# Kernel optimization log

Measured on AMD Instinct MI355X. Metric: run time of the kernel, lower is better.

The kernel has to match this reference:

```python
import jax, jax.numpy as jnp
import numpy as np

N = 100000   # nodes
E = 1000000  # edges
G = 1024     # graphs
S = 128      # subgraphs (super-graphs)
NODE = 64    # node feature dim
EDGE = 32    # edge feature dim
H = 64       # hidden size
OUT = 32     # output classes
L = 3        # num GIN layers
BN_EPS = 1e-5


def setup_inputs() -> dict:
    key = jax.random.key(0)
    ks = jax.random.split(key, 32)
    p = lambda k, shape: jax.random.normal(k, shape, jnp.float32) * 0.05
    inp = {
        "x": jax.random.normal(ks[0], (N, NODE), jnp.float32),
        "edge_index": jax.random.randint(ks[1], (2, E), 0, N),
        "edge_attr": jax.random.normal(ks[2], (E, EDGE), jnp.float32),
        "batch": jnp.sort(jax.random.randint(ks[3], (N,), 0, G)),
        "weights": jax.random.uniform(ks[4], (G, 1), jnp.float32, 0.1, 1.0),
        "subgraph_batch": jnp.sort(jax.random.randint(ks[5], (G,), 0, S)),
        # per-layer GINConv params (node_size == hidden_size so layers stack)
        "be_w1": p(ks[6], (L, EDGE, H)), "be_b1": p(ks[7], (L, H)),
        "be_w2": p(ks[8], (L, H, H)),   "be_b2": p(ks[9], (L, H)),
        "mlp_w1": p(ks[10], (L, H, H)), "mlp_b1": p(ks[11], (L, H)),
        "mlp_w2": p(ks[12], (L, H, H)), "mlp_b2": p(ks[13], (L, H)),
        "eps": jnp.zeros((L,), jnp.float32),
        "bn_gamma": jnp.ones((L, H), jnp.float32),
        "bn_beta": jnp.zeros((L, H), jnp.float32),
        "fc0_w": p(ks[14], (L * H, H)), "fc0_b": p(ks[15], (H,)),
        "fc1_w": p(ks[16], (H, H)),     "fc1_b": p(ks[17], (H,)),
        "fc2_w": p(ks[18], (H, H)),     "fc2_b": p(ks[19], (H,)),
        "pred_w": p(ks[20], (H, OUT)),  "pred_b": p(ks[21], (OUT,)),
    }
    return inp


def reference(x, edge_index, edge_attr, batch, weights, subgraph_batch,
              be_w1, be_b1, be_w2, be_b2, mlp_w1, mlp_b1, mlp_w2, mlp_b2,
              eps, bn_gamma, bn_beta, fc0_w, fc0_b, fc1_w, fc1_b,
              fc2_w, fc2_b, pred_w, pred_b):
    src, dst = edge_index[0], edge_index[1]
    n = x.shape[0]
    h = x
    xs = []
    for l in range(be_w1.shape[0]):
        # bond encoder: Linear -> ReLU -> Linear  [E, H]
        e = jnp.maximum(edge_attr @ be_w1[l] + be_b1[l], 0.0) @ be_w2[l] + be_b2[l]
        # message: relu(x_j + edge_emb), aggregate: scatter-add to target nodes
        msg = jnp.maximum(h[src] + e, 0.0)                      # [E, H]
        agg = jax.ops.segment_sum(msg, dst, num_segments=n)     # [N, H]
        z = (1.0 + eps[l]) * h + agg
        # update MLP: Linear -> ReLU -> Linear, then outer ReLU
        z = jnp.maximum(z @ mlp_w1[l] + mlp_b1[l], 0.0) @ mlp_w2[l] + mlp_b2[l]
        z = jnp.maximum(z, 0.0)
        # BatchNorm over nodes (training-mode batch statistics, biased var)
        mu = z.mean(axis=0)
        var = z.var(axis=0)
        z = (z - mu) * jax.lax.rsqrt(var + BN_EPS) * bn_gamma[l] + bn_beta[l]
        h = z
        xs.append(z)
    hc = jnp.concatenate(xs, axis=-1)                           # [N, L*H]
    g_num = weights.shape[0]
    cnt = jax.ops.segment_sum(jnp.ones((n,), hc.dtype), batch, num_segments=g_num)
    g = jax.ops.segment_sum(hc, batch, num_segments=g_num) / jnp.maximum(cnt, 1.0)[:, None]
    g = jnp.maximum(g @ fc0_w + fc0_b, 0.0) * weights           # [G, H]
    s = jax.ops.segment_sum(g, subgraph_batch, num_segments=S)  # [S, H]
    norm = jax.ops.segment_sum(weights, subgraph_batch, num_segments=S)
    s = s / jnp.maximum(norm, 1e-12)
    s = jnp.maximum(s @ fc1_w + fc1_b, 0.0)
    s = jnp.maximum(s @ fc2_w + fc2_b, 0.0)
    return s @ pred_w + pred_b                                  # [S, OUT]
```

## Files before the change

### kernel.cpp

```cpp
#include <hip/hip_runtime.h>

#define NN 100000
#define NE 1000000
#define NG 1024
#define NSG 128
#define EF 32
#define HH 64
#define NOUT 32
#define NL 3
#define NWAVE (NE / 64)
#define NGRP_N (NN / 16)

typedef __attribute__((ext_vector_type(8))) short bf16x8;
typedef __attribute__((ext_vector_type(4))) float f32x4;

#define EMIDX(row, c) ((row) * 64 + (((c) + (row) * 4) & 63))

__device__ __forceinline__ float bcastf(float v, int l) {
    return __int_as_float(__builtin_amdgcn_readlane(__float_as_int(v), l));
}

__device__ __forceinline__ short f2bf(float x) {
    unsigned u = __float_as_uint(x);
    u += 0x7FFFu + ((u >> 16) & 1u);
    return (short)(u >> 16);
}

__device__ __forceinline__ float bf2f(short h) {
    return __uint_as_float(((unsigned)(unsigned short)h) << 16);
}

__device__ __forceinline__ void wave_lds_sync() {
    __builtin_amdgcn_wave_barrier();
    asm volatile("s_waitcnt lgkmcnt(0)" ::: "memory");
    __builtin_amdgcn_wave_barrier();
}

__device__ __forceinline__ void gld16(const float* g, float* l) {
    __builtin_amdgcn_global_load_lds(
        (const __attribute__((address_space(1))) void*)g,
        (__attribute__((address_space(3))) void*)l, 16, 0, 0);
}

#define WAITVM_(n) asm volatile("s_waitcnt vmcnt(" #n ")" ::: "memory")
#define WAITVM(n) WAITVM_(n)

__global__ void prep_kernel(const int* __restrict__ batch, const int* __restrict__ sgb,
                            const float* __restrict__ w,
                            float* __restrict__ cnt, float* __restrict__ norm) {
    int i = blockIdx.x * blockDim.x + threadIdx.x;
    if (i < NN) atomicAdd(&cnt[batch[i]], 1.0f);
    if (i < NG) atomicAdd(&norm[sgb[i]], w[i]);
}

__global__ void hist_kernel(const int* __restrict__ eidx, int* __restrict__ off) {
    int e = blockIdx.x * 256 + threadIdx.x;
    if (e < NE) atomicAdd(&off[eidx[NE + e]], 1);
}

__global__ void scan1(int* __restrict__ off, int* __restrict__ bsum) {
    __shared__ int s[256];
    const int i = blockIdx.x * 256 + threadIdx.x;
    const int v = (i < NN) ? off[i] : 0;
    s[threadIdx.x] = v; __syncthreads();
    for (int d = 1; d < 256; d <<= 1) {
        const int t = (threadIdx.x >= d) ? s[threadIdx.x - d] : 0;
        __syncthreads(); s[threadIdx.x] += t; __syncthreads();
    }
    if (i < NN) off[i] = s[threadIdx.x] - v;
    if (threadIdx.x == 255) bsum[blockIdx.x] = s[255];
}

__global__ void scan2(int* __restrict__ bsum, int nb) {
    __shared__ int s[512];
    const int v = (threadIdx.x < nb) ? bsum[threadIdx.x] : 0;
    s[threadIdx.x] = v; __syncthreads();
    for (int d = 1; d < 512; d <<= 1) {
        const int t = (threadIdx.x >= d) ? s[threadIdx.x - d] : 0;
        __syncthreads(); s[threadIdx.x] += t; __syncthreads();
    }
    if (threadIdx.x < nb) bsum[threadIdx.x] = s[threadIdx.x] - v;
}

__global__ void scan3(int* __restrict__ off, const int* __restrict__ bsum) {
    const int i = blockIdx.x * 256 + threadIdx.x;
    if (i < NN) off[i] += bsum[blockIdx.x];
}

__global__ void scatter_kernel(const int* __restrict__ eidx, int* __restrict__ off,
                               int* __restrict__ perm_s, int* __restrict__ src_s,
                               int* __restrict__ dst_s) {
    int e = blockIdx.x * 256 + threadIdx.x;
    if (e < NE) {
        const int d = eidx[NE + e];
        const int p = atomicAdd(&off[d], 1);
        perm_s[p] = e;
        src_s[p]  = eidx[e];
        dst_s[p]  = d;
    }
}

__global__ __launch_bounds__(256, 4) void edge_mfma(
    const float* __restrict__ hin,
    const float* __restrict__ eattr,
    const int*   __restrict__ perm_s,
    const int*   __restrict__ src_s,
    const int*   __restrict__ dst_s,
    const float* __restrict__ w1,
    const float* __restrict__ b1,
    const float* __restrict__ w2,
    const float* __restrict__ b2,
    float*       __restrict__ agg)
{
    __shared__ float ldsall[4][2560];
    const int lane = threadIdx.x & 63;
    const int wv   = threadIdx.x >> 6;
    const int col  = lane & 15;
    const int quad = lane >> 4;
    float* EM = &ldsall[wv][0];
    short* T  = (short*)EM;
    float* HG = &ldsall[wv][1024];
    float* EA = &ldsall[wv][2048];

    const int wid = __builtin_amdgcn_readfirstlane(
        (blockIdx.x * 256 + (int)threadIdx.x) >> 6);
    if (wid >= NWAVE) return;
    const int ebase = wid * 64;

    bf16x8 B1f[4];
    #pragma unroll
    for (int nt = 0; nt < 4; ++nt)
        #pragma unroll
        for (int j = 0; j < 8; ++j)
            B1f[nt][j] = f2bf(w1[(quad * 8 + j) * HH + nt * 16 + col]);
    bf16x8 B2f[2][4];
    #pragma unroll
    for (int ks = 0; ks < 2; ++ks)
        #pragma unroll
        for (int nt = 0; nt < 4; ++nt)
            #pragma unroll
            for (int j = 0; j < 8; ++j)
                B2f[ks][nt][j] = f2bf(w2[(ks * 32 + quad * 8 + j) * HH + nt * 16 + col]);
    float b1v[4], b2v[4];
    #pragma unroll
    for (int nt = 0; nt < 4; ++nt) {
        b1v[nt] = b1[nt * 16 + col];
        b2v[nt] = b2[nt * 16 + col];
    }

    const int sv_all = src_s[ebase + lane];
    const int dv_all = dst_s[ebase + lane];
    const int pe_all = perm_s[ebase + lane];

    const int ea_srcchunk = (lane & 7) ^ ((lane >> 3) & 7);
    const int ea_subrow   = lane >> 3;
    const int hg_subrow   = lane >> 4;
    const int hg_off      = (lane & 15) * 4;

    #define ISSUE_EA(g)                                                        \
        {                                                                      \
            _Pragma("unroll")                                                  \
            for (int b = 0; b < 2; ++b) {                                      \
                const int srow = (g) * 16 + b * 8 + ea_subrow;                 \
                const int pe   = __shfl(pe_all, srow, 64);                     \
                gld16(eattr + (size_t)pe * EF + ea_srcchunk * 4,               \
                      EA + b * 256);                                           \
            }                                                                  \
        }
    #define ISSUE_HG(g)                                                        \
        {                                                                      \
            _Pragma("unroll")                                                  \
            for (int b = 0; b < 4; ++b) {                                      \
                const int srow = (g) * 16 + b * 4 + hg_subrow;                 \
                const int s    = __shfl(sv_all, srow, 64);                     \
                gld16(hin + (size_t)s * HH + hg_off, HG + b * 256);            \
            }                                                                  \
        }

    WAITVM(0);
    __builtin_amdgcn_sched_barrier(0);

    ISSUE_EA(0);
    ISSUE_HG(0);

    int   cur = -1;
    float acc = 0.0f;

    #pragma unroll
    for (int gi = 0; gi < 4; ++gi) {
        WAITVM(4);
        __builtin_amdgcn_sched_barrier(0);

        const int sbase = (2 * quad) ^ (col & 6);
        const float4 fa = *(const float4*)&EA[col * 32 + sbase * 4];
        const float4 fb = *(const float4*)&EA[col * 32 + sbase * 4 + 4];
        const bool odd = (col & 1);
        const float4 lo = odd ? fb : fa;
        const float4 hi = odd ? fa : fb;
        bf16x8 A1;
        A1[0] = f2bf(lo.x); A1[1] = f2bf(lo.y); A1[2] = f2bf(lo.z); A1[3] = f2bf(lo.w);
        A1[4] = f2bf(hi.x); A1[5] = f2bf(hi.y); A1[6] = f2bf(hi.z); A1[7] = f2bf(hi.w);
        wave_lds_sync();
        if (gi < 3) ISSUE_EA(gi + 1);

        #pragma unroll
        for (int nt = 0; nt < 4; ++nt) {
            f32x4 C = {0.f, 0.f, 0.f, 0.f};
            C = __builtin_amdgcn_mfma_f32_16x16x32_bf16(A1, B1f[nt], C, 0, 0, 0);
            #pragma unroll
            for (int r = 0; r < 4; ++r) {
                const float tv = fmaxf(C[r] + b1v[nt], 0.0f);
                T[(quad * 4 + r) * 72 + nt * 16 + col] = f2bf(tv);
            }
        }
        wave_lds_sync();

        bf16x8 A2_0 = *(const bf16x8*)&T[col * 72 + 0  + quad * 8];
        bf16x8 A2_1 = *(const bf16x8*)&T[col * 72 + 32 + quad * 8];
        wave_lds_sync();

        #pragma unroll
        for (int nt = 0; nt < 4; ++nt) {
            f32x4 C = {0.f, 0.f, 0.f, 0.f};
            C = __builtin_amdgcn_mfma_f32_16x16x32_bf16(A2_0, B2f[0][nt], C, 0, 0, 0);
            C = __builtin_amdgcn_mfma_f32_16x16x32_bf16(A2_1, B2f[1][nt], C, 0, 0, 0);
            #pragma unroll
            for (int r = 0; r < 4; ++r)
                EM[EMIDX(quad * 4 + r, nt * 16 + col)] = C[r] + b2v[nt];
        }
        wave_lds_sync();

        if (gi < 3) { WAITVM(2); } else { WAITVM(0); }
        __builtin_amdgcn_sched_barrier(0);

        #pragma unroll
        for (int e2 = 0; e2 < 16; ++e2) {
            const int d = __builtin_amdgcn_readlane(dv_all, gi * 16 + e2);
            const float msg = fmaxf(HG[e2 * 64 + lane] + EM[EMIDX(e2, lane)], 0.0f);
            if (d != cur) {
                if (cur >= 0) atomicAdd(&agg[(size_t)cur * HH + lane], acc);
                acc = 0.0f; cur = d;
            }
            acc += msg;
        }
        wave_lds_sync();
        if (gi < 3) ISSUE_HG(gi + 1);
    }
    if (cur >= 0) atomicAdd(&agg[(size_t)cur * HH + lane], acc);
    #undef ISSUE_EA
    #undef ISSUE_HG
}

__global__ __launch_bounds__(256, 3) void node_mfma(
    const float* __restrict__ hin,
    float*       agg,
    const float* __restrict__ w1, const float* __restrict__ b1,
    const float* __restrict__ w2, const float* __restrict__ b2,
    const float* __restrict__ epsp,
    float*       __restrict__ stats)
{
    __shared__ short wt[4][64 * 72];
    __shared__ float em[4][16 * 64];

    const int tid = threadIdx.x;
    for (int idx = tid; idx < HH * HH; idx += 256) {
        const int k = idx >> 6, n = idx & 63;
        {
            const float w = w1[idx];
            const short h = f2bf(w);
            wt[0][n * 72 + k] = h;
            wt[1][n * 72 + k] = f2bf(w - bf2f(h));
        }
        {
            const float w = w2[idx];
            const short h = f2bf(w);
            wt[2][n * 72 + k] = h;
            wt[3][n * 72 + k] = f2bf(w - bf2f(h));
        }
    }
    __syncthreads();

    const int lane = tid & 63;
    const int wv   = tid >> 6;
    const int col  = lane & 15;
    const int quad = lane >> 4;
    float* EM = em[wv];
    const float epsv = 1.0f + epsp[0];
    const int wid = blockIdx.x * 4 + wv;

    float b1v[4], b2v[4];
    #pragma unroll
    for (int nt = 0; nt < 4; ++nt) {
        b1v[nt] = b1[nt * 16 + col];
        b2v[nt] = b2[nt * 16 + col];
    }

    float s1 = 0.0f, s2 = 0.0f;

    #pragma unroll 1
    for (int gi = 0; gi < 4; ++gi) {
        const int grp = wid * 4 + gi;
        if (grp >= NGRP_N) break;
        const int n0  = grp * 16;
        const int row = n0 + col;

        bf16x8 Ah[2], Al[2];
        #pragma unroll
        for (int ks = 0; ks < 2; ++ks) {
            const float* hp = hin + (size_t)row * HH + ks * 32 + quad * 8;
            const float* gp = agg + (size_t)row * HH + ks * 32 + quad * 8;
            const float4 h0 = *(const float4*)hp;
            const float4 h1 = *(const float4*)(hp + 4);
            const float4 g0 = *(const float4*)gp;
            const float4 g1 = *(const float4*)(gp + 4);
            float z[8];
            z[0] = fmaf(epsv, h0.x, g0.x); z[1] = fmaf(epsv, h0.y, g0.y);
            z[2] = fmaf(epsv, h0.z, g0.z); z[3] = fmaf(epsv, h0.w, g0.w);
            z[4] = fmaf(epsv, h1.x, g1.x); z[5] = fmaf(epsv, h1.y, g1.y);
            z[6] = fmaf(epsv, h1.z, g1.z); z[7] = fmaf(epsv, h1.w, g1.w);
            #pragma unroll
            for (int j = 0; j < 8; ++j) {
                const short h = f2bf(z[j]);
                Ah[ks][j] = h;
                Al[ks][j] = f2bf(z[j] - bf2f(h));
            }
        }

        #pragma unroll
        for (int nt = 0; nt < 4; ++nt) {
            f32x4 C = {0.f, 0.f, 0.f, 0.f};
            #pragma unroll
            for (int ks = 0; ks < 2; ++ks) {
                const int wo = (nt * 16 + col) * 72 + ks * 32 + quad * 8;
                const bf16x8 Bh = *(const bf16x8*)&wt[0][wo];
                const bf16x8 Bl = *(const bf16x8*)&wt[1][wo];
                C = __builtin_amdgcn_mfma_f32_16x16x32_bf16(Ah[ks], Bh, C, 0, 0, 0);
                C = __builtin_amdgcn_mfma_f32_16x16x32_bf16(Al[ks], Bh, C, 0, 0, 0);
                C = __builtin_amdgcn_mfma_f32_16x16x32_bf16(Ah[ks], Bl, C, 0, 0, 0);
            }
            #pragma unroll
            for (int r = 0; r < 4; ++r)
                EM[EMIDX(quad * 4 + r, nt * 16 + col)] = fmaxf(C[r] + b1v[nt], 0.0f);
        }
        wave_lds_sync();

        bf16x8 Th[2], Tl[2];
        #pragma unroll
        for (int ks = 0; ks < 2; ++ks) {
            const int c0 = (ks * 32 + quad * 8 + col * 4) & 63;
            const float* tp = &EM[col * 64 + c0];
            const float4 t0 = *(const float4*)tp;
            const int c1 = (ks * 32 + quad * 8 + 4 + col * 4) & 63;
            const float4 t1 = *(const float4*)&EM[col * 64 + c1];
            float tz[8] = {t0.x, t0.y, t0.z, t0.w, t1.x, t1.y, t1.z, t1.w};
            #pragma unroll
            for (int j = 0; j < 8; ++j) {
                const short h = f2bf(tz[j]);
                Th[ks][j] = h;
                Tl[ks][j] = f2bf(tz[j] - bf2f(h));
            }
        }
        wave_lds_sync();

        #pragma unroll
        for (int nt = 0; nt < 4; ++nt) {
            f32x4 C = {0.f, 0.f, 0.f, 0.f};
            #pragma unroll
            for (int ks = 0; ks < 2; ++ks) {
                const int wo = (nt * 16 + col) * 72 + ks * 32 + quad * 8;
                const bf16x8 Bh = *(const bf16x8*)&wt[2][wo];
                const bf16x8 Bl = *(const bf16x8*)&wt[3][wo];
                C = __builtin_amdgcn_mfma_f32_16x16x32_bf16(Th[ks], Bh, C, 0, 0, 0);
                C = __builtin_amdgcn_mfma_f32_16x16x32_bf16(Tl[ks], Bh, C, 0, 0, 0);
                C = __builtin_amdgcn_mfma_f32_16x16x32_bf16(Th[ks], Bl, C, 0, 0, 0);
            }
            #pragma unroll
            for (int r = 0; r < 4; ++r)
                EM[EMIDX(quad * 4 + r, nt * 16 + col)] = fmaxf(C[r] + b2v[nt], 0.0f);
        }
        wave_lds_sync();

        #pragma unroll 4
        for (int e2 = 0; e2 < 16; ++e2) {
            const float val = EM[EMIDX(e2, lane)];
            agg[(size_t)(n0 + e2) * HH + lane] = val;
            s1 += val;
            s2 += val * val;
        }
        wave_lds_sync();
    }
    atomicAdd(&stats[lane], s1);
    atomicAdd(&stats[64 + lane], s2);
}

#define CHUNK 32
__global__ void bn_apply(
    const float* __restrict__ v, const float* __restrict__ stats,
    const float* __restrict__ gamma, const float* __restrict__ beta,
    const int* __restrict__ batch,
    float* __restrict__ hout, float* __restrict__ pooled, int layer)
{
    const int lane = threadIdx.x & 63;
    const int wv   = (blockIdx.x * blockDim.x + threadIdx.x) >> 6;
    const int n0   = wv * CHUNK;
    if (n0 >= NN) return;
    const int n1 = min(n0 + CHUNK, NN);
    const float mu  = stats[lane] * (1.0f / NN);
    const float var = stats[64 + lane] * (1.0f / NN) - mu * mu;
    const float rs  = 1.0f / sqrtf(var + 1e-5f);
    const float ga = gamma[lane],       be = beta[lane];
    float acc = 0.0f;
    int cur = batch[n0];
    for (int n = n0; n < n1; ++n) {
        const int b = batch[n];
        const float z = (v[(size_t)n * HH + lane] - mu) * rs * ga + be;
        hout[(size_t)n * HH + lane] = z;
        if (b != cur) {
            atomicAdd(&pooled[(size_t)cur * (NL * HH) + layer * HH + lane], acc);
            acc = 0.0f; cur = b;
        }
        acc += z;
    }
    atomicAdd(&pooled[(size_t)cur * (NL * HH) + layer * HH + lane], acc);
}

__global__ __launch_bounds__(256, 1) void graph_kernel(
    const float* __restrict__ pooled, const float* __restrict__ cnt,
    const float* __restrict__ fc0_w, const float* __restrict__ fc0_b,
    const float* __restrict__ wts, const int* __restrict__ sgb,
    float* __restrict__ s_acc)
{
    __shared__ float w[NL * HH * HH];
    for (int i = threadIdx.x; i < NL * HH * HH; i += blockDim.x) w[i] = fc0_w[i];
    __syncthreads();
    const int lane = threadIdx.x & 63;
    const int g = blockIdx.x * 4 + (threadIdx.x >> 6);
    if (g >= NG) return;
    const float inv = 1.0f / fmaxf(cnt[g], 1.0f);
    float acc = fc0_b[lane];
    #pragma unroll
    for (int c = 0; c < NL; ++c) {
        const float a = pooled[g * (NL * HH) + c * HH + lane] * inv;
        #pragma unroll
        for (int k = 0; k < HH; ++k)
            acc = fmaf(bcastf(a, k), w[(c * HH + k) * HH + lane], acc);
    }
    const float og = fmaxf(acc, 0.0f) * wts[g];
    atomicAdd(&s_acc[sgb[g] * HH + lane], og);
}

__global__ __launch_bounds__(256, 1) void final_kernel(
    const float* __restrict__ s_acc, const float* __restrict__ norm,
    const float* __restrict__ fc1_w, const float* __restrict__ fc1_b,
    const float* __restrict__ fc2_w, const float* __restrict__ fc2_b,
    const float* __restrict__ pw, const float* __restrict__ pb,
    float* __restrict__ out)
{
    const int lane = threadIdx.x & 63;
    const int s = blockIdx.x * 4 + (threadIdx.x >> 6);
    if (s >= NSG) return;
    const float xv = s_acc[s * HH + lane] / fmaxf(norm[s], 1e-12f);
    float u = fc1_b[lane];
    #pragma unroll
    for (int k = 0; k < HH; ++k) u = fmaf(bcastf(xv, k), fc1_w[k * HH + lane], u);
    u = fmaxf(u, 0.0f);
    float v = fc2_b[lane];
    #pragma unroll
    for (int k = 0; k < HH; ++k) v = fmaf(bcastf(u, k), fc2_w[k * HH + lane], v);
    v = fmaxf(v, 0.0f);
    float o = pb[lane & 31];
    #pragma unroll
    for (int k = 0; k < HH; ++k) o = fmaf(bcastf(v, k), pw[k * NOUT + (lane & 31)], o);
    if (lane < NOUT) out[s * NOUT + lane] = o;
}

extern "C" void kernel_launch(void* const* d_in, const int* in_sizes, int n_in,
                              void* d_out, int out_size, void* d_ws, size_t ws_size,
                              hipStream_t stream)
{
    const float* x        = (const float*)d_in[0];
    const int*   eidx     = (const int*)d_in[1];
    const float* eattr    = (const float*)d_in[2];
    const int*   batch    = (const int*)d_in[3];
    const float* weights  = (const float*)d_in[4];
    const int*   sgb      = (const int*)d_in[5];
    const float* be_w1    = (const float*)d_in[6];
    const float* be_b1    = (const float*)d_in[7];
    const float* be_w2    = (const float*)d_in[8];
    const float* be_b2    = (const float*)d_in[9];
    const float* mlp_w1   = (const float*)d_in[10];
    const float* mlp_b1   = (const float*)d_in[11];
    const float* mlp_w2   = (const float*)d_in[12];
    const float* mlp_b2   = (const float*)d_in[13];
    const float* eps      = (const float*)d_in[14];
    const float* bn_gamma = (const float*)d_in[15];
    const float* bn_beta  = (const float*)d_in[16];
    const float* fc0_w    = (const float*)d_in[17];
    const float* fc0_b    = (const float*)d_in[18];
    const float* fc1_w    = (const float*)d_in[19];
    const float* fc1_b    = (const float*)d_in[20];
    const float* fc2_w    = (const float*)d_in[21];
    const float* fc2_b    = (const float*)d_in[22];
    const float* pred_w   = (const float*)d_in[23];
    const float* pred_b   = (const float*)d_in[24];
    float* out = (float*)d_out;

    float* ws     = (float*)d_ws;
    float* h_buf  = ws;
    float* agg    = ws + (size_t)NN * HH;
    float* stats  = ws + (size_t)NN * HH * 2;
    float* pooled = stats + 256;
    float* cnt    = pooled + (size_t)NG * NL * HH;
    float* s_acc  = cnt + NG;
    float* norm   = s_acc + (size_t)NSG * HH;
    int*   ioff   = (int*)(norm + NSG);
    int*   bsum   = ioff + NN;
    int*   perm_s = bsum + 512;
    int*   src_s  = perm_s + NE;
    int*   dst_s  = src_s + NE;

    size_t acc_floats = (size_t)NG * NL * HH + NG + (size_t)NSG * HH + NSG;
    hipMemsetAsync(pooled, 0, acc_floats * sizeof(float), stream);
    hipMemsetAsync(ioff, 0, NN * sizeof(int), stream);

    const int nb = (NN + 255) / 256;
    hist_kernel<<<(NE + 255) / 256, 256, 0, stream>>>(eidx, ioff);
    scan1<<<nb, 256, 0, stream>>>(ioff, bsum);
    scan2<<<1, 512, 0, stream>>>(bsum, nb);
    scan3<<<nb, 256, 0, stream>>>(ioff, bsum);
    scatter_kernel<<<(NE + 255) / 256, 256, 0, stream>>>(eidx, ioff, perm_s, src_s, dst_s);

    prep_kernel<<<(NN + 255) / 256, 256, 0, stream>>>(batch, sgb, weights, cnt, norm);

    const float* hin = x;
    const int eblocks = (NWAVE + 3) / 4;
    const int node_blocks = (NGRP_N + 15) / 16;
    const int bn_waves  = (NN + CHUNK - 1) / CHUNK;
    const int bn_blocks = (bn_waves + 3) / 4;
    for (int l = 0; l < NL; ++l) {
        hipMemsetAsync(agg, 0, ((size_t)NN * HH + 256) * sizeof(float), stream);
        edge_mfma<<<eblocks, 256, 0, stream>>>(
            hin, eattr, perm_s, src_s, dst_s,
            be_w1 + l * EF * HH, be_b1 + l * HH,
            be_w2 + l * HH * HH, be_b2 + l * HH, agg);
        node_mfma<<<node_blocks, 256, 0, stream>>>(
            hin, agg,
            mlp_w1 + l * HH * HH, mlp_b1 + l * HH,
            mlp_w2 + l * HH * HH, mlp_b2 + l * HH,
            eps + l, stats);
        bn_apply<<<bn_blocks, 256, 0, stream>>>(
            agg, stats, bn_gamma + l * HH, bn_beta + l * HH,
            batch, h_buf, pooled, l);
        hin = h_buf;
    }

    graph_kernel<<<NG / 4, 256, 0, stream>>>(pooled, cnt, fc0_w, fc0_b,
                                             weights, sgb, s_acc);
    final_kernel<<<NSG / 4, 256, 0, stream>>>(s_acc, norm, fc1_w, fc1_b,
                                              fc2_w, fc2_b, pred_w, pred_b, out);
}
```

Measured before the change: 908.2 us.

## Remap edge blocks per XCD, pad LDS rows, fold agg clearing into bn_apply

Result: faster. 849.0 us (-6.5%).

```diff
diff --git a/kernel.cpp b/kernel.cpp
--- a/kernel.cpp
+++ b/kernel.cpp
@@ -10,6 +10,7 @@
 #define NL 3
 #define NWAVE (NE / 64)
 #define NGRP_N (NN / 16)
+#define EBLOCKS ((NWAVE + 3) / 4)
 
 typedef __attribute__((ext_vector_type(8))) short bf16x8;
 typedef __attribute__((ext_vector_type(4))) float f32x4;
@@ -112,18 +113,23 @@
     const float* __restrict__ b2,
     float*       __restrict__ agg)
 {
-    __shared__ float ldsall[4][2560];
+    __shared__ float ldsall[4][2624];
     const int lane = threadIdx.x & 63;
     const int wv   = threadIdx.x >> 6;
     const int col  = lane & 15;
     const int quad = lane >> 4;
     float* EM = &ldsall[wv][0];
     short* T  = (short*)EM;
-    float* HG = &ldsall[wv][1024];
-    float* EA = &ldsall[wv][2048];
+    float* HG = &ldsall[wv][1088];
+    float* EA = &ldsall[wv][2112];
+
+    const int bid = blockIdx.x;
+    const int xcd = bid & 7, loc = bid >> 3;
+    const int q = EBLOCKS >> 3, r = EBLOCKS & 7;
+    const int sbid = (xcd < r ? xcd * (q + 1) : r * (q + 1) + (xcd - r) * q) + loc;
 
     const int wid = __builtin_amdgcn_readfirstlane(
-        (blockIdx.x * 256 + (int)threadIdx.x) >> 6);
+        (sbid * 256 + (int)threadIdx.x) >> 6);
     if (wid >= NWAVE) return;
     const int ebase = wid * 64;
 
@@ -226,7 +232,7 @@
             C = __builtin_amdgcn_mfma_f32_16x16x32_bf16(A2_1, B2f[1][nt], C, 0, 0, 0);
             #pragma unroll
             for (int r = 0; r < 4; ++r)
-                EM[EMIDX(quad * 4 + r, nt * 16 + col)] = C[r] + b2v[nt];
+                EM[(quad * 4 + r) * 68 + nt * 16 + col] = C[r] + b2v[nt];
         }
         wave_lds_sync();
 
@@ -236,7 +242,7 @@
         #pragma unroll
         for (int e2 = 0; e2 < 16; ++e2) {
             const int d = __builtin_amdgcn_readlane(dv_all, gi * 16 + e2);
-            const float msg = fmaxf(HG[e2 * 64 + lane] + EM[EMIDX(e2, lane)], 0.0f);
+            const float msg = fmaxf(HG[e2 * 64 + lane] + EM[e2 * 68 + lane], 0.0f);
             if (d != cur) {
                 if (cur >= 0) atomicAdd(&agg[(size_t)cur * HH + lane], acc);
                 acc = 0.0f; cur = d;
@@ -348,8 +354,7 @@
         #pragma unroll
         for (int ks = 0; ks < 2; ++ks) {
             const int c0 = (ks * 32 + quad * 8 + col * 4) & 63;
-            const float* tp = &EM[col * 64 + c0];
-            const float4 t0 = *(const float4*)tp;
+            const float4 t0 = *(const float4*)&EM[col * 64 + c0];
             const int c1 = (ks * 32 + quad * 8 + 4 + col * 4) & 63;
             const float4 t1 = *(const float4*)&EM[col * 64 + c1];
             float tz[8] = {t0.x, t0.y, t0.z, t0.w, t1.x, t1.y, t1.z, t1.w};
@@ -395,10 +400,11 @@
 
 #define CHUNK 32
 __global__ void bn_apply(
-    const float* __restrict__ v, const float* __restrict__ stats,
+    const float* __restrict__ v, float* __restrict__ aggz,
+    const float* __restrict__ stats,
     const float* __restrict__ gamma, const float* __restrict__ beta,
     const int* __restrict__ batch,
-    float* __restrict__ hout, float* __restrict__ pooled, int layer)
+    float* __restrict__ hout, float* __restrict__ pooled, int layer, int clr)
 {
     const int lane = threadIdx.x & 63;
     const int wv   = (blockIdx.x * blockDim.x + threadIdx.x) >> 6;
@@ -415,6 +421,7 @@
         const int b = batch[n];
         const float z = (v[(size_t)n * HH + lane] - mu) * rs * ga + be;
         hout[(size_t)n * HH + lane] = z;
+        if (clr) aggz[(size_t)n * HH + lane] = 0.0f;
         if (b != cur) {
             atomicAdd(&pooled[(size_t)cur * (NL * HH) + layer * HH + lane], acc);
             acc = 0.0f; cur = b;
@@ -508,10 +515,10 @@
     float* ws     = (float*)d_ws;
     float* h_buf  = ws;
     float* agg    = ws + (size_t)NN * HH;
-    float* stats  = ws + (size_t)NN * HH * 2;
-    float* pooled = stats + 256;
+    float* pooled = ws + (size_t)NN * HH * 2;
     float* cnt    = pooled + (size_t)NG * NL * HH;
-    float* s_acc  = cnt + NG;
+    float* stats  = cnt + NG;
+    float* s_acc  = stats + NL * 128;
     float* norm   = s_acc + (size_t)NSG * HH;
     int*   ioff   = (int*)(norm + NSG);
     int*   bsum   = ioff + NN;
@@ -519,8 +526,9 @@
     int*   src_s  = perm_s + NE;
     int*   dst_s  = src_s + NE;
 
-    size_t acc_floats = (size_t)NG * NL * HH + NG + (size_t)NSG * HH + NSG;
+    size_t acc_floats = (size_t)NG * NL * HH + NG + NL * 128 + (size_t)NSG * HH + NSG;
     hipMemsetAsync(pooled, 0, acc_floats * sizeof(float), stream);
+    hipMemsetAsync(agg, 0, (size_t)NN * HH * sizeof(float), stream);
     hipMemsetAsync(ioff, 0, NN * sizeof(int), stream);
 
     const int nb = (NN + 255) / 256;
@@ -533,13 +541,11 @@
     prep_kernel<<<(NN + 255) / 256, 256, 0, stream>>>(batch, sgb, weights, cnt, norm);
 
     const float* hin = x;
-    const int eblocks = (NWAVE + 3) / 4;
     const int node_blocks = (NGRP_N + 15) / 16;
     const int bn_waves  = (NN + CHUNK - 1) / CHUNK;
     const int bn_blocks = (bn_waves + 3) / 4;
     for (int l = 0; l < NL; ++l) {
-        hipMemsetAsync(agg, 0, ((size_t)NN * HH + 256) * sizeof(float), stream);
-        edge_mfma<<<eblocks, 256, 0, stream>>>(
+        edge_mfma<<<EBLOCKS, 256, 0, stream>>>(
             hin, eattr, perm_s, src_s, dst_s,
             be_w1 + l * EF * HH, be_b1 + l * HH,
             be_w2 + l * HH * HH, be_b2 + l * HH, agg);
@@ -547,10 +553,10 @@
             hin, agg,
             mlp_w1 + l * HH * HH, mlp_b1 + l * HH,
             mlp_w2 + l * HH * HH, mlp_b2 + l * HH,
-            eps + l, stats);
+            eps + l, stats + l * 128);
         bn_apply<<<bn_blocks, 256, 0, stream>>>(
-            agg, stats, bn_gamma + l * HH, bn_beta + l * HH,
-            batch, h_buf, pooled, l);
+            agg, agg, stats + l * 128, bn_gamma + l * HH, bn_beta + l * HH,
+            batch, h_buf, pooled, l, (l < NL - 1) ? 1 : 0);
         hin = h_buf;
     }
 
```
